# Performance work log

Measured on AMD Instinct MI355X. Metric: run time of the kernel, lower is better.

Reference implementation:

```python
import jax, jax.numpy as jnp
import numpy as np
from jax import lax

ROUTING_ITERS = 3
EPS = 1e-8


def _conv(x, w, b, stride=1):
    # x: [B,C,H,W], w: [O,C,kh,kw]  (VALID padding, NCHW/OIHW)
    y = lax.conv_general_dilated(x, w, (stride, stride), 'VALID',
                                 dimension_numbers=('NCHW', 'OIHW', 'NCHW'))
    return y + b[None, :, None, None]


def _maxpool2(x):
    return lax.reduce_window(x, -jnp.inf, lax.max, (1, 1, 2, 2), (1, 1, 2, 2), 'VALID')


def _squash(s, axis=-1):
    n2 = jnp.sum(s * s, axis=axis, keepdims=True)
    return s * (n2 / (1.0 + n2)) / jnp.sqrt(n2 + EPS)


def setup_inputs() -> dict:
    key = jax.random.key(0)
    ks = jax.random.split(key, 9)
    p = lambda k, shp: (jax.random.normal(k, shp, dtype=jnp.float32) * 0.05)
    return {
        'x':  jax.random.normal(ks[0], (64, 1, 92, 92), dtype=jnp.float32),
        'w1': p(ks[1], (128, 1, 9, 9)),   'b1': jnp.zeros((128,), jnp.float32),
        'w2': p(ks[2], (64, 128, 5, 5)),  'b2': jnp.zeros((64,), jnp.float32),
        'wc': p(ks[3], (128, 64, 8, 8)),  'bc': jnp.zeros((128,), jnp.float32),
        # routing transform: [num_primary=1024, num_sar=10, out_dim=16, in_dim=32]
        'Wr': p(ks[4], (1024, 10, 16, 32)),
    }


def reference(x, w1, b1, w2, b2, wc, bc, Wr):
    B = x.shape[0]
    # feature extractor (dropout is identity at inference)
    h = jax.nn.relu(_conv(x, w1, b1))          # [B,128,84,84]
    h = _maxpool2(h)                            # [B,128,42,42]
    h = _conv(h, w2, b2)                        # [B,64,38,38]
    # primary capsule conv
    h = _conv(h, wc, bc, stride=2)              # [B,128,16,16]
    # 128 channels = 4 capsule types * 32-dim capsules, 16x16 spatial -> 1024 caps
    u = h.reshape(B, 4, 32, 16, 16).transpose(0, 1, 3, 4, 2).reshape(B, 1024, 32)
    u = _squash(u)                              # [B,1024,32]
    # u_hat: predictions of each primary cap for each SAR cap
    u_hat = jnp.einsum('bpi,ptoi->bpto', u, Wr)  # [B,1024,10,16]
    # dynamic routing
    b_log = jnp.zeros((B, 1024, 10), dtype=x.dtype)
    for _ in range(ROUTING_ITERS):
        c = jax.nn.softmax(b_log, axis=2)               # [B,1024,10]
        s = jnp.einsum('bpt,bpto->bto', c, u_hat)       # [B,10,16]
        v = _squash(s)                                   # [B,10,16]
        b_log = b_log + jnp.einsum('bpto,bto->bpt', u_hat, v)
    likelihood = jnp.sqrt(jnp.sum(v * v, axis=-1) + EPS)  # [B,10]
    return likelihood
```

## Files before the change

kernel.cpp:

```cpp
#include <hip/hip_runtime.h>
#include <hip/hip_bf16.h>
#include <math.h>


#define EPSF 1e-8f

typedef __bf16 bf16x8 __attribute__((ext_vector_type(8)));
typedef __bf16 bf16x4 __attribute__((ext_vector_type(4)));
typedef float floatx4 __attribute__((ext_vector_type(4)));
typedef float floatx16 __attribute__((ext_vector_type(16)));

__global__ __launch_bounds__(256) void k_t_w1b(const float* __restrict__ w1, __bf16* __restrict__ w1b) {
    int i = blockIdx.x * 256 + threadIdx.x;
    if (i >= 12288) return;
    int kt = i >> 10, oc = (i >> 3) & 127, j = i & 7;
    int k = kt * 8 + j;
    w1b[i] = (__bf16)(k < 81 ? w1[oc * 81 + k] : 0.f);
}

__global__ __launch_bounds__(256) void k_t_w2a(const float* __restrict__ w2, __bf16* __restrict__ w2a) {
    int i = blockIdx.x * 256 + threadIdx.x;
    if (i >= 204800) return;
    int j = i & 7, lane = (i >> 3) & 63, f = i >> 9;
    int mt = f & 1, ks = (f >> 1) & 3, rem = f >> 3;
    int khw = rem % 25, icc = rem / 25;
    int c32 = lane & 31, h = lane >> 5;
    int oc = mt * 32 + c32;
    int ic = icc * 64 + ks * 16 + h * 8 + j;
    w2a[i] = (__bf16)w2[(oc * 128 + ic) * 25 + khw];
}

__global__ __launch_bounds__(256) void k_t_wca(const float* __restrict__ wc, __bf16* __restrict__ wca) {
    int i = blockIdx.x * 256 + threadIdx.x;
    if (i >= 524288) return;
    int j = i & 7, lane = (i >> 3) & 63, f = i >> 9;
    int ct = f & 3, ks = (f >> 2) & 1, khw = (f >> 3) & 63, icc = f >> 9;
    int c32 = lane & 31, h = lane >> 5;
    int oc = ct * 32 + c32;
    int ic = icc * 32 + ks * 16 + h * 8 + j;
    wca[i] = (__bf16)wc[(oc * 64 + ic) * 64 + khw];
}

__global__ __launch_bounds__(256) void k_t_wrb(const float* __restrict__ Wr, __bf16* __restrict__ wrb) {
    int i = blockIdx.x * 256 + threadIdx.x;
    if (i >= 5242880) return;
    wrb[i] = (__bf16)Wr[i];
}

__global__ __launch_bounds__(256, 3) void k_conv1_mfma(const float* __restrict__ x,
                                                       const __bf16* __restrict__ w1b,
                                                       const float* __restrict__ b1,
                                                       __bf16* __restrict__ h1n) {
    __shared__ float xs[960];
    __shared__ __bf16 Bl[18432];
    int py = blockIdx.x, ocg = blockIdx.y, b = blockIdx.z;
    int t = threadIdx.x;
    int lane = t & 63, w = t >> 6;
    int cc = lane & 15, q = lane >> 4;

    const float* xb = x + (size_t)b * 8464 + 2 * py * 92;
    for (int j = t; j < 920; j += 256) xs[j] = xb[j];

    int ocA = ocg * 64 + w * 16 + cc;
    bf16x8 af[3];
#pragma unroll
    for (int ks = 0; ks < 3; ++ks)
        af[ks] = *(const bf16x8*)(w1b + ((ks * 4 + q) * 128 + ocA) * 8);

    __syncthreads();

    if (t < 192) {
        int row = t / 96, pos = t - (t / 96) * 96;
        int sbase = row * 92 + pos;
        bool pvalid = pos < 84;
#pragma unroll
        for (int kt = 0; kt < 12; ++kt) {
            bf16x8 pk;
#pragma unroll
            for (int j = 0; j < 8; ++j) {
                int k = kt * 8 + j;
                int kh = k / 9, kw = k - kh * 9;
                float v = (pvalid && k < 81) ? xs[sbase + kh * 92 + kw] : 0.f;
                pk[j] = (__bf16)v;
            }
            *(bf16x8*)(Bl + ((kt * 2 + row) * 96 + pos) * 8) = pk;
        }
    }
    __syncthreads();

    floatx4 acc[2][6];
    const char* Bb = (const char*)Bl + cc * 16 + q * 3072;
#pragma unroll
    for (int rr = 0; rr < 2; ++rr)
#pragma unroll
        for (int n6 = 0; n6 < 6; ++n6) {
            floatx4 a = (floatx4){0.f, 0.f, 0.f, 0.f};
#pragma unroll
            for (int ks = 0; ks < 3; ++ks) {
                bf16x8 bf = *(const bf16x8*)(Bb + ks * 12288 + rr * 1536 + n6 * 256);
                a = __builtin_amdgcn_mfma_f32_16x16x32_bf16(af[ks], bf, a, 0, 0, 0);
            }
            acc[rr][n6] = a;
        }

    int oc0 = ocg * 64 + w * 16 + q * 4;
    float4 bv = *(const float4*)(b1 + oc0);
    size_t obase = (((size_t)b * 42 + py) * 42) * 128 + oc0;
#pragma unroll
    for (int n6 = 0; n6 < 6; ++n6) {
        bf16x4 pk;
#pragma unroll
        for (int r = 0; r < 4; ++r) {
            float vert = fmaxf(acc[0][n6][r], acc[1][n6][r]);
            float hz = fmaxf(vert, __shfl_xor(vert, 1, 64));
            float pooled = fmaxf(hz + ((const float*)&bv)[r], 0.f);
            pk[r] = (__bf16)pooled;
        }
        if ((cc & 1) == 0) {
            int px = n6 * 8 + (cc >> 1);
            if (px < 42)
                *(bf16x4*)(h1n + obase + (size_t)px * 128) = pk;
        }
    }
}

__global__ __launch_bounds__(192, 2) void k_conv2(const __bf16* __restrict__ h1n,
                                                  const __bf16* __restrict__ w2a,
                                                  float* __restrict__ p01) {
    __shared__ __bf16 ins[25704];
    int g = blockIdx.x, b = blockIdx.y, icc = blockIdx.z;
    int row0 = g * 5;
    int t = threadIdx.x;
    int lane = t & 63, w = t >> 6;
    int c32 = lane & 31, h = lane >> 5;
    int validp = (g < 7) ? 190 : 114;
    int ic0 = icc * 64;

    int baseN[2], posi[2];
#pragma unroll
    for (int nt = 0; nt < 2; ++nt) {
        int pi = (w * 2 + nt) * 32 + c32;
        int pc = pi < validp ? pi : validp - 1;
        int r = pc / 38, c = pc - r * 38;
        posi[nt] = pi;
        baseN[nt] = (r * 42 + c) * 136 + h * 16;
    }

#pragma unroll
    for (int half = 0; half < 2; ++half) {
        uint4 rb[8];
        int lo[8];
#pragma unroll
        for (int k = 0; k < 8; ++k) {
            int j = (half * 8 + k) * 192 + t;
            if (j > 3023) j -= 192;
            int lr = j / 336, rem = j - lr * 336;
            int ix = rem >> 3, sb = rem & 7;
            int rg = row0 + lr; if (rg > 41) rg = 41;
            rb[k] = *(const uint4*)(h1n + ((((size_t)b * 42 + rg) * 42 + ix) * 128 + ic0 + sb * 8));
            lo[k] = (lr * 42 + ix) * 136 + sb * 16;
        }
#pragma unroll
        for (int k = 0; k < 8; ++k)
            *(uint4*)((char*)ins + lo[k]) = rb[k];
    }

    floatx16 acc[2][2];
#pragma unroll
    for (int mt = 0; mt < 2; ++mt)
#pragma unroll
        for (int nt = 0; nt < 2; ++nt)
#pragma unroll
            for (int i = 0; i < 16; ++i) acc[mt][nt][i] = 0.f;

    __syncthreads();
    const __bf16* wic = w2a + (size_t)icc * 25 * 4096 + (lane << 3);
#pragma unroll
    for (int khw = 0; khw < 25; ++khw) {
        int kh = khw / 5, kw = khw - kh * 5;
        int doff = (kh * 42 + kw) * 136;
        const __bf16* wk = wic + khw * 4096;
#pragma unroll
        for (int ks = 0; ks < 4; ++ks) {
            bf16x8 a0 = *(const bf16x8*)(wk + ks * 1024);
            bf16x8 a1 = *(const bf16x8*)(wk + ks * 1024 + 512);
#pragma unroll
            for (int nt = 0; nt < 2; ++nt) {
                bf16x8 bfr = *(const bf16x8*)((char*)ins + baseN[nt] + doff + ks * 32);
                acc[0][nt] = __builtin_amdgcn_mfma_f32_32x32x16_bf16(a0, bfr, acc[0][nt], 0, 0, 0);
                acc[1][nt] = __builtin_amdgcn_mfma_f32_32x32x16_bf16(a1, bfr, acc[1][nt], 0, 0, 0);
            }
        }
    }
    float* pdst = p01 + (size_t)icc * 5914624;
#pragma unroll
    for (int nt = 0; nt < 2; ++nt) {
        int pi = posi[nt];
        if (pi < validp) {
            int r = pi / 38, c = pi - r * 38;
            int oh = row0 + r;
            size_t obase = (((size_t)b * 38 + oh) * 38 + c) * 64;
#pragma unroll
            for (int mt = 0; mt < 2; ++mt) {
#pragma unroll
                for (int g2 = 0; g2 < 4; ++g2) {
                    int oc0 = mt * 32 + g2 * 8 + h * 4;
                    floatx4 pv;
                    pv[0] = acc[mt][nt][g2 * 4 + 0];
                    pv[1] = acc[mt][nt][g2 * 4 + 1];
                    pv[2] = acc[mt][nt][g2 * 4 + 2];
                    pv[3] = acc[mt][nt][g2 * 4 + 3];
                    *(floatx4*)(pdst + obase + oc0) = pv;
                }
            }
        }
    }
}

__global__ __launch_bounds__(256) void k_reduce_h2(const float* __restrict__ p01,
                                                   const float* __restrict__ b2,
                                                   __bf16* __restrict__ h2n) {
    int i = blockIdx.x * 256 + threadIdx.x;
    if (i >= 1478656) return;
    size_t e = (size_t)i * 4;
    floatx4 a = *(const floatx4*)(p01 + e);
    floatx4 b = *(const floatx4*)(p01 + 5914624 + e);
    floatx4 bv = *(const floatx4*)(b2 + ((i * 4) & 63));
    bf16x4 pk;
    pk.x = (__bf16)(a[0] + b[0] + bv[0]);
    pk.y = (__bf16)(a[1] + b[1] + bv[1]);
    pk.z = (__bf16)(a[2] + b[2] + bv[2]);
    pk.w = (__bf16)(a[3] + b[3] + bv[3]);
    *(bf16x4*)(h2n + e) = pk;
}

__global__ __launch_bounds__(256, 4) void k_convcaps(const __bf16* __restrict__ h2n,
                                                     const __bf16* __restrict__ wca,
                                                     const float* __restrict__ bc,
                                                     __bf16* __restrict__ ub) {
    __shared__ __bf16 ins[13680];
    int g = blockIdx.x, b = blockIdx.y;
    int t = threadIdx.x;
    int lane = t & 63, ct = t >> 6;
    int c32 = lane & 31, h = lane >> 5;
    int rloc = c32 >> 4, cx = c32 & 15;

    floatx16 acc;
#pragma unroll
    for (int i = 0; i < 16; ++i) acc[i] = 0.f;

    int Bbase = (76 * rloc + cx) * 72 + h * 16;
    for (int icc = 0; icc < 2; ++icc) {
        int ic0 = icc * 32;
        __syncthreads();
        {
            uint4 rb[6];
            int lo[6];
#pragma unroll
            for (int k = 0; k < 6; ++k) {
                int j = k * 256 + t;
                if (j > 1519) j -= 256;
                int r = j / 152, rem = j - r * 152;
                int c = rem >> 2, s = rem & 3;
                rb[k] = *(const uint4*)(h2n + ((((size_t)b * 38 + 4 * g + r) * 38 + c) * 64 + ic0 + s * 8));
                int X = (r * 2 + (c & 1)) * 19 + (c >> 1);
                lo[k] = X * 72 + s * 16;
            }
#pragma unroll
            for (int k = 0; k < 6; ++k)
                *(uint4*)((char*)ins + lo[k]) = rb[k];
        }
        __syncthreads();
        const __bf16* wic = wca + ((size_t)icc * 64 * 8 + ct) * 512 + (lane << 3);
#pragma unroll
        for (int khw = 0; khw < 64; ++khw) {
            int kh = khw >> 3, kw = khw & 7;
            int par = kw & 1, k2 = kw >> 1;
            int doff = ((kh * 2 + par) * 19 + k2) * 72;
            const __bf16* wk = wic + khw * 4096;
#pragma unroll
            for (int ks = 0; ks < 2; ++ks) {
                bf16x8 af = *(const bf16x8*)(wk + ks * 2048);
                bf16x8 bfr = *(const bf16x8*)((char*)ins + Bbase + doff + ks * 32);
                acc = __builtin_amdgcn_mfma_f32_32x32x16_bf16(af, bfr, acc, 0, 0, 0);
            }
        }
    }
    float vals[16];
    float n2p = 0.f;
#pragma unroll
    for (int g2 = 0; g2 < 4; ++g2) {
        float4 bv = *(const float4*)(bc + ct * 32 + g2 * 8 + h * 4);
#pragma unroll
        for (int j = 0; j < 4; ++j) {
            float v = acc[g2 * 4 + j] + ((const float*)&bv)[j];
            vals[g2 * 4 + j] = v;
            n2p = fmaf(v, v, n2p);
        }
    }
    float n2 = n2p + __shfl_xor(n2p, 32, 64);
    float scale = (n2 / (1.f + n2)) / sqrtf(n2 + EPSF);
    int pos = (2 * g + rloc) * 16 + cx;
    __bf16* dst = ub + (((size_t)b * 1024 + ct * 256 + pos) * 32);
#pragma unroll
    for (int g2 = 0; g2 < 4; ++g2) {
        bf16x4 pk;
        pk.x = (__bf16)(vals[g2 * 4 + 0] * scale);
        pk.y = (__bf16)(vals[g2 * 4 + 1] * scale);
        pk.z = (__bf16)(vals[g2 * 4 + 2] * scale);
        pk.w = (__bf16)(vals[g2 * 4 + 3] * scale);
        *(bf16x4*)(dst + g2 * 8 + h * 4) = pk;
    }
}

__global__ __launch_bounds__(256, 2) void k_uhat(const __bf16* __restrict__ ub,
                                                 const __bf16* __restrict__ wrb,
                                                 __bf16* __restrict__ uhT) {
    int pt = blockIdx.x, ts = blockIdx.y, bz = blockIdx.z;
    int t = threadIdx.x;
    int p = pt * 64 + (t & 63);
    int q = t >> 6;
    bf16x8 wf[4][4];
#pragma unroll
    for (int o4 = 0; o4 < 4; ++o4)
#pragma unroll
        for (int j = 0; j < 4; ++j)
            wf[o4][j] = *(const bf16x8*)(wrb + (((size_t)p * 10 + ts) * 16 + q * 4 + o4) * 32 + j * 8);
#pragma unroll 1
    for (int bi = 0; bi < 16; ++bi) {
        int b = bz * 16 + bi;
        bf16x8 uf[4];
        const bf16x8* up = (const bf16x8*)(ub + ((size_t)b * 1024 + p) * 32);
#pragma unroll
        for (int j = 0; j < 4; ++j) uf[j] = up[j];
#pragma unroll
        for (int o4 = 0; o4 < 4; ++o4) {
            float s = 0.f;
#pragma unroll
            for (int j = 0; j < 4; ++j)
#pragma unroll
                for (int e = 0; e < 8; ++e)
                    s = fmaf((float)uf[j][e], (float)wf[o4][j][e], s);
            uhT[(((size_t)b * 10 + ts) * 16 + q * 4 + o4) * 1024 + p] = (__bf16)s;
        }
    }
}

__global__ __launch_bounds__(256) void k_route_s(const __bf16* __restrict__ uhT,
                                                 const float* __restrict__ bl,
                                                 float* __restrict__ vout,
                                                 float* __restrict__ out,
                                                 int first, int last) {
    __shared__ float sred[4][16];
    int b = blockIdx.x, tt = blockIdx.y;
    int t = threadIdx.x;
    float acc[16];
#pragma unroll
    for (int o = 0; o < 16; ++o) acc[o] = 0.f;
    const float* blb = bl + b * 10240;
    const __bf16* uhb = uhT + ((size_t)b * 10 + tt) * 16384;
    for (int p = t; p < 1024; p += 256) {
        float c;
        if (first) {
            c = 0.1f;
        } else {
            float den = 0.f, et = 0.f;
#pragma unroll
            for (int tp = 0; tp < 10; ++tp) {
                float e = expf(blb[tp * 1024 + p]);
                den += e;
                if (tp == tt) et = e;
            }
            c = et / den;
        }
#pragma unroll
        for (int o = 0; o < 16; ++o)
            acc[o] = fmaf(c, (float)uhb[o * 1024 + p], acc[o]);
    }
    int lane = t & 63, wid = t >> 6;
#pragma unroll
    for (int o = 0; o < 16; ++o) {
        float v = acc[o];
#pragma unroll
        for (int off = 32; off >= 1; off >>= 1) v += __shfl_xor(v, off, 64);
        if (lane == 0) sred[wid][o] = v;
    }
    __syncthreads();
    if (t < 16) {
        float s = (sred[0][t] + sred[1][t]) + (sred[2][t] + sred[3][t]);
        float n2 = s * s;
#pragma unroll
        for (int off = 1; off < 16; off <<= 1) n2 += __shfl_xor(n2, off, 16);
        float scale = (n2 / (1.f + n2)) / sqrtf(n2 + EPSF);
        vout[(b * 10 + tt) * 16 + t] = s * scale;
        if (last && t == 0) {
            float sv2 = n2 * scale * scale;
            out[b * 10 + tt] = sqrtf(sv2 + EPSF);
        }
    }
}

__global__ __launch_bounds__(256) void k_route_b(const __bf16* __restrict__ uhT,
                                                 const float* __restrict__ vv,
                                                 float* __restrict__ bl,
                                                 int first) {
    __shared__ float vs[16];
    int b = blockIdx.x, tt = blockIdx.y;
    int t = threadIdx.x;
    if (t < 16) vs[t] = vv[(b * 10 + tt) * 16 + t];
    __syncthreads();
    const __bf16* uhb = uhT + ((size_t)b * 10 + tt) * 16384;
    float* blb = bl + (b * 10 + tt) * 1024;
    for (int p = t; p < 1024; p += 256) {
        float d = 0.f;
#pragma unroll
        for (int o = 0; o < 16; ++o) d = fmaf((float)uhb[o * 1024 + p], vs[o], d);
        blb[p] = first ? d : (blb[p] + d);
    }
}

extern "C" void kernel_launch(void* const* d_in, const int* in_sizes, int n_in,
                              void* d_out, int out_size, void* d_ws, size_t ws_size,
                              hipStream_t stream) {
    const float* x  = (const float*)d_in[0];
    const float* w1 = (const float*)d_in[1];
    const float* b1 = (const float*)d_in[2];
    const float* w2 = (const float*)d_in[3];
    const float* b2 = (const float*)d_in[4];
    const float* wc = (const float*)d_in[5];
    const float* bc = (const float*)d_in[6];
    const float* Wr = (const float*)d_in[7];
    float* out = (float*)d_out;
    float* ws  = (float*)d_ws;

    __bf16* w2a = (__bf16*)(ws);
    __bf16* wca = (__bf16*)(ws + 102400);
    __bf16* w1b = (__bf16*)(ws + 364544);
    __bf16* h1n = (__bf16*)(ws + 375040);
    __bf16* h2n = (__bf16*)(ws + 7600384);
    __bf16* ub  = (__bf16*)(ws + 12654848);
    float*  bl  = ws + 14752000;
    float*  vv  = ws + 15407360;
    __bf16* wrb = (__bf16*)(ws + 15417600);
    float*  p01 = ws + 18039040;
    __bf16* uhT = (__bf16*)(ws + 375040);

    k_t_w1b<<<48, 256, 0, stream>>>(w1, w1b);
    k_t_w2a<<<800, 256, 0, stream>>>(w2, w2a);
    k_t_wca<<<2048, 256, 0, stream>>>(wc, wca);
    k_t_wrb<<<20480, 256, 0, stream>>>(Wr, wrb);
    k_conv1_mfma<<<dim3(42, 2, 64), 256, 0, stream>>>(x, w1b, b1, h1n);
    k_conv2<<<dim3(8, 64, 2), 192, 0, stream>>>(h1n, w2a, p01);
    k_reduce_h2<<<5776, 256, 0, stream>>>(p01, b2, h2n);
    k_convcaps<<<dim3(8, 64), 256, 0, stream>>>(h2n, wca, bc, ub);
    k_uhat<<<dim3(16, 10, 4), 256, 0, stream>>>(ub, wrb, uhT);
    k_route_s<<<dim3(64, 10), 256, 0, stream>>>(uhT, bl, vv, out, 1, 0);
    k_route_b<<<dim3(64, 10), 256, 0, stream>>>(uhT, vv, bl, 1);
    k_route_s<<<dim3(64, 10), 256, 0, stream>>>(uhT, bl, vv, out, 0, 0);
    k_route_b<<<dim3(64, 10), 256, 0, stream>>>(uhT, vv, bl, 0);
    k_route_s<<<dim3(64, 10), 256, 0, stream>>>(uhT, bl, vv, out, 0, 1);
}
```

Before: 324.0 us.

## Fuse routing agreement and coupling kernels with LDS-cached predictions and ping-pong logits

Merges the per-iteration routing-sum kernel and the logit-update kernel into one kernel. Each block stages its 32 KB u_hat slice in shared memory once and reuses it for both the weighted sum and the agreement dot product. The squashed vector stays in shared memory instead of going through global memory. Logits ping-pong between two buffers so blocks reading the softmax inputs never race with writers. This cuts the routing launches from five to three and halves u_hat global reads, at the cost of higher LDS use per block and an extra workspace buffer.

```diff
diff --git a/kernel.cpp b/kernel.cpp
--- a/kernel.cpp
+++ b/kernel.cpp
@@ -346,19 +346,28 @@
     }
 }
 
-__global__ __launch_bounds__(256) void k_route_s(const __bf16* __restrict__ uhT,
-                                                 const float* __restrict__ bl,
-                                                 float* __restrict__ vout,
-                                                 float* __restrict__ out,
-                                                 int first, int last) {
+__global__ __launch_bounds__(256) void k_route(const __bf16* __restrict__ uhT,
+                                               const float* __restrict__ blR,
+                                               float* __restrict__ blW,
+                                               float* __restrict__ out,
+                                               int first, int dob, int last) {
+    __shared__ __bf16 uh_s[16384];
     __shared__ float sred[4][16];
+    __shared__ float vs[16];
     int b = blockIdx.x, tt = blockIdx.y;
     int t = threadIdx.x;
+    const __bf16* uhb = uhT + ((size_t)b * 10 + tt) * 16384;
+#pragma unroll
+    for (int k = 0; k < 8; ++k) {
+        int j = k * 256 + t;
+        *(uint4*)((char*)uh_s + j * 16) = *(const uint4*)((const char*)uhb + j * 16);
+    }
+    __syncthreads();
+
     float acc[16];
 #pragma unroll
     for (int o = 0; o < 16; ++o) acc[o] = 0.f;
-    const float* blb = bl + b * 10240;
-    const __bf16* uhb = uhT + ((size_t)b * 10 + tt) * 16384;
+    const float* blb = blR + b * 10240;
     for (int p = t; p < 1024; p += 256) {
         float c;
         if (first) {
@@ -375,7 +384,7 @@
         }
 #pragma unroll
         for (int o = 0; o < 16; ++o)
-            acc[o] = fmaf(c, (float)uhb[o * 1024 + p], acc[o]);
+            acc[o] = fmaf(c, (float)uh_s[o * 1024 + p], acc[o]);
     }
     int lane = t & 63, wid = t >> 6;
 #pragma unroll
@@ -392,30 +401,23 @@
 #pragma unroll
         for (int off = 1; off < 16; off <<= 1) n2 += __shfl_xor(n2, off, 16);
         float scale = (n2 / (1.f + n2)) / sqrtf(n2 + EPSF);
-        vout[(b * 10 + tt) * 16 + t] = s * scale;
+        vs[t] = s * scale;
         if (last && t == 0) {
             float sv2 = n2 * scale * scale;
             out[b * 10 + tt] = sqrtf(sv2 + EPSF);
         }
     }
-}
-
-__global__ __launch_bounds__(256) void k_route_b(const __bf16* __restrict__ uhT,
-                                                 const float* __restrict__ vv,
-                                                 float* __restrict__ bl,
-                                                 int first) {
-    __shared__ float vs[16];
-    int b = blockIdx.x, tt = blockIdx.y;
-    int t = threadIdx.x;
-    if (t < 16) vs[t] = vv[(b * 10 + tt) * 16 + t];
-    __syncthreads();
-    const __bf16* uhb = uhT + ((size_t)b * 10 + tt) * 16384;
-    float* blb = bl + (b * 10 + tt) * 1024;
-    for (int p = t; p < 1024; p += 256) {
-        float d = 0.f;
-#pragma unroll
-        for (int o = 0; o < 16; ++o) d = fmaf((float)uhb[o * 1024 + p], vs[o], d);
-        blb[p] = first ? d : (blb[p] + d);
+    __syncthreads();
+
+    if (dob) {
+        const float* blr = blR + (b * 10 + tt) * 1024;
+        float* blw = blW + (b * 10 + tt) * 1024;
+        for (int p = t; p < 1024; p += 256) {
+            float d = 0.f;
+#pragma unroll
+            for (int o = 0; o < 16; ++o) d = fmaf((float)uh_s[o * 1024 + p], vs[o], d);
+            blw[p] = first ? d : (blr[p] + d);
+        }
     }
 }
 
@@ -439,10 +441,10 @@
     __bf16* h1n = (__bf16*)(ws + 375040);
     __bf16* h2n = (__bf16*)(ws + 7600384);
     __bf16* ub  = (__bf16*)(ws + 12654848);
-    float*  bl  = ws + 14752000;
-    float*  vv  = ws + 15407360;
+    float*  blA = ws + 14752000;
     __bf16* wrb = (__bf16*)(ws + 15417600);
     float*  p01 = ws + 18039040;
+    float*  blB = ws + 29868288;
     __bf16* uhT = (__bf16*)(ws + 375040);
 
     k_t_w1b<<<48, 256, 0, stream>>>(w1, w1b);
@@ -454,9 +456,7 @@
     k_reduce_h2<<<5776, 256, 0, stream>>>(p01, b2, h2n);
     k_convcaps<<<dim3(8, 64), 256, 0, stream>>>(h2n, wca, bc, ub);
     k_uhat<<<dim3(16, 10, 4), 256, 0, stream>>>(ub, wrb, uhT);
-    k_route_s<<<dim3(64, 10), 256, 0, stream>>>(uhT, bl, vv, out, 1, 0);
-    k_route_b<<<dim3(64, 10), 256, 0, stream>>>(uhT, vv, bl, 1);
-    k_route_s<<<dim3(64, 10), 256, 0, stream>>>(uhT, bl, vv, out, 0, 0);
-    k_route_b<<<dim3(64, 10), 256, 0, stream>>>(uhT, vv, bl, 0);
-    k_route_s<<<dim3(64, 10), 256, 0, stream>>>(uhT, bl, vv, out, 0, 1);
-}
+    k_route<<<dim3(64, 10), 256, 0, stream>>>(uhT, blA, blA, out, 1, 1, 0);
+    k_route<<<dim3(64, 10), 256, 0, stream>>>(uhT, blA, blB, out, 0, 1, 0);
+    k_route<<<dim3(64, 10), 256, 0, stream>>>(uhT, blB, blB, out, 0, 0, 1);
+}
```

Result: faster. 315.2 us (-2.7%).
